# Optimization experiments

Hardware: AMD Instinct MI355X
Metric: run time of the kernel (lower is better)

## Reference

```python
import jax, jax.numpy as jnp
import numpy as np

B, L = 8, 2048
D_MODEL = 512
D_INNER = 1024   # expand * d_model
D_STATE = 16
D_CONV = 4
DT_RANK = 32     # d_model // 16
N_EXPERT = 4     # num_expert - 1 real experts (id 0 = identity)
N_LAYER = 2      # num_mamba_layer


def setup_inputs() -> dict:
    key = jax.random.key(0)
    ks = jax.random.split(key, 12)
    def rn(k, shape, scale):
        return jax.random.normal(k, shape, jnp.float32) * scale
    P = (N_EXPERT, N_LAYER)
    A_log = jnp.broadcast_to(
        jnp.log(jnp.arange(1, D_STATE + 1, dtype=jnp.float32)),
        P + (D_INNER, D_STATE)).copy()
    return {
        "x": rn(ks[0], (B, L, D_MODEL), 1.0),
        "expert_id": jax.random.randint(ks[1], (B,), 0, N_EXPERT + 1, jnp.int32),
        "W_in": rn(ks[2], P + (D_MODEL, 2 * D_INNER), D_MODEL ** -0.5),
        "conv_w": rn(ks[3], P + (D_INNER, D_CONV), D_CONV ** -0.5),
        "conv_b": jnp.zeros(P + (D_INNER,), jnp.float32),
        "W_x": rn(ks[4], P + (D_INNER, DT_RANK + 2 * D_STATE), D_INNER ** -0.5),
        "W_dt": rn(ks[5], P + (DT_RANK, D_INNER), DT_RANK ** -0.5),
        "b_dt": rn(ks[6], P + (D_INNER,), 0.1) - 4.0,  # softplus -> small dt
        "A_log": A_log,
        "D": jnp.ones(P + (D_INNER,), jnp.float32),
        "W_out": rn(ks[7], P + (D_INNER, D_MODEL), D_INNER ** -0.5),
    }


def _mamba_block(x, W_in, conv_w, conv_b, W_x, W_dt, b_dt, A_log, Dp, W_out):
    # x: [L, D_MODEL]
    Lx = x.shape[0]
    xr = x @ W_in                               # [L, 2*D_INNER]
    xc, res = jnp.split(xr, 2, axis=-1)
    # causal depthwise conv (kernel D_CONV), left-padded
    xp = jnp.pad(xc, ((D_CONV - 1, 0), (0, 0)))
    xc = sum(xp[k:k + Lx] * conv_w[:, k] for k in range(D_CONV)) + conv_b
    xc = jax.nn.silu(xc)
    proj = xc @ W_x                             # [L, DT_RANK + 2*D_STATE]
    dt = jax.nn.softplus(proj[:, :DT_RANK] @ W_dt + b_dt)        # [L, D_INNER]
    Bm = proj[:, DT_RANK:DT_RANK + D_STATE]                      # [L, D_STATE]
    Cm = proj[:, DT_RANK + D_STATE:]                             # [L, D_STATE]
    A = -jnp.exp(A_log)                                          # [D_INNER, D_STATE]
    def step(h, t):
        dt_t, B_t, C_t, x_t = t
        # discretize inside the step to avoid materializing [L,D_INNER,D_STATE]
        h = jnp.exp(dt_t[:, None] * A) * h + (dt_t * x_t)[:, None] * B_t[None, :]
        return h, h @ C_t                                        # y_t: [D_INNER]
    h0 = jnp.zeros((D_INNER, D_STATE), dtype=x.dtype)
    _, ys = jax.lax.scan(step, h0, (dt, Bm, Cm, xc))
    y = ys + Dp * xc
    y = y * jax.nn.silu(res)
    return y @ W_out                                             # [L, D_MODEL]


def reference(x, expert_id, W_in, conv_w, conv_b, W_x, W_dt, b_dt, A_log, D, W_out):
    # expert_id==0 -> identity; otherwise run expert (expert_id-1)'s stacked blocks
    idx = jnp.clip(expert_id - 1, 0, N_EXPERT - 1)
    def per_sample(xi, e):
        out = xi
        for l in range(N_LAYER):
            out = _mamba_block(out, W_in[e, l], conv_w[e, l], conv_b[e, l],
                               W_x[e, l], W_dt[e, l], b_dt[e, l],
                               A_log[e, l], D[e, l], W_out[e, l])
        return out
    y = jax.vmap(per_sample)(x, idx)
    return jnp.where((expert_id == 0)[:, None, None], x, y)
```

## Files before the change

kernel.cpp:

```cpp
#include <hip/hip_runtime.h>
#include <hip/hip_bf16.h>
#include <cmath>

#define B_SZ 8
#define L_SZ 2048
#define DM 512
#define DI 1024
#define DS 16
#define DC 4
#define DTR 32
#define NE 4
#define NL 2
#define NCH 64
#define TC2 32
#define TPER 8

typedef __attribute__((ext_vector_type(8))) short bf16x8;
typedef __attribute__((ext_vector_type(8))) unsigned short u16x8;
typedef __attribute__((ext_vector_type(4))) float f32x4;

__device__ __forceinline__ unsigned short f2bf(float x) {
  __hip_bfloat16 h = __float2bfloat16(x);
  return __builtin_bit_cast(unsigned short, h);
}
__device__ __forceinline__ float bf2f(unsigned short u) {
  return __builtin_bit_cast(float, (unsigned)u << 16);
}

__device__ __forceinline__ void glds16(const unsigned short* g, unsigned short* l) {
  __builtin_amdgcn_global_load_lds(
      (const __attribute__((address_space(1))) unsigned int*)g,
      (__attribute__((address_space(3))) unsigned int*)l, 16, 0, 0);
}

__device__ __forceinline__ float softplus_fast(float v) {
  return (v > 20.f) ? v : __logf(1.f + __expf(v));
}

__device__ __forceinline__ void pow16(float g, float* ee) {
  float g2 = g * g, g4 = g2 * g2, g8 = g4 * g4;
  ee[0] = g;        ee[1] = g2;       ee[2] = g2 * g;   ee[3] = g4;
  ee[4] = g4 * g;   ee[5] = g4 * g2;  ee[6] = ee[5] * g; ee[7] = g8;
  ee[8] = g8 * g;   ee[9] = g8 * g2;  ee[10] = ee[9] * g; ee[11] = g8 * g4;
  ee[12] = ee[11] * g; ee[13] = ee[11] * g2; ee[14] = ee[13] * g; ee[15] = g8 * g8;
}

__global__ __launch_bounds__(256) void transpose_w_kernel(
    const float* __restrict__ in, unsigned short* __restrict__ out, int R, int C)
{
  __shared__ float t[32][33];
  const int p = blockIdx.z;
  const int r0 = blockIdx.y * 32, c0 = blockIdx.x * 32;
  const int tx = threadIdx.x & 31, ty = threadIdx.x >> 5;
  const float* ip = in + (long)p * R * C;
  unsigned short* op = out + (long)p * R * C;
  #pragma unroll
  for (int i = 0; i < 32; i += 8)
    t[ty + i][tx] = ip[(long)(r0 + ty + i) * C + c0 + tx];
  __syncthreads();
  #pragma unroll
  for (int i = 0; i < 32; i += 8)
    op[(long)(c0 + ty + i) * R + r0 + tx] = f2bf(t[tx][ty + i]);
}

__global__ __launch_bounds__(256) void f2bf_kernel(
    const float* __restrict__ in, unsigned short* __restrict__ out)
{
  long i = ((long)blockIdx.x * 256 + threadIdx.x) * 4;
  float4 v = *(const float4*)(in + i);
  out[i + 0] = f2bf(v.x); out[i + 1] = f2bf(v.y);
  out[i + 2] = f2bf(v.z); out[i + 3] = f2bf(v.w);
}

template<int EPI, int TM, int TN>
__global__ __launch_bounds__(256) void gemm_bf16(
    const unsigned short* __restrict__ Abase, long aBatch, int K, int lda,
    const unsigned short* __restrict__ WTbase, long wStride,
    const float* __restrict__ xpass,
    const int* __restrict__ expert_id, int layer,
    float* __restrict__ Cf, unsigned short* __restrict__ Cbh,
    unsigned short* __restrict__ Cbh2,
    int ldc, long cBatch)
{
  constexpr int IF = TM / 32;
  constexpr int JF = TN / 32;
  constexpr int AST = TM / 4;
  constexpr int BST = TN / 4;

  const int b = blockIdx.z;
  const int eid = expert_id[b];
  const int m0 = blockIdx.y * TM, n0 = blockIdx.x * TN;
  const int tid = threadIdx.x;

  if (eid == 0) {
    if (EPI == 2) {
      float* Co = Cf + (long)b * cBatch;
      const float* xp = xpass + (long)b * L_SZ * DM;
      for (int i = tid; i < TM * TN; i += 256) {
        int r = m0 + (i / TN), c = n0 + (i % TN);
        Co[(long)r * ldc + c] = xp[(long)r * DM + c];
      }
    }
    return;
  }
  const int e = min(max(eid - 1, 0), NE - 1);
  const unsigned short* A = Abase + (long)b * aBatch;
  const unsigned short* WT = WTbase + (long)(e * NL + layer) * wStride;

  __shared__ unsigned short As[TM * 64];
  __shared__ unsigned short Bs[TN * 64];

  const int w = tid >> 6, lane = tid & 63;
  const int srow = lane >> 2;
  const int sgsw = ((lane & 3) ^ ((srow >> 1) & 3)) * 8;

  const unsigned short* aG0 = A + (long)(m0 + w * AST + srow) * lda + sgsw;
  const unsigned short* aG1 = aG0 + 16 * lda;
  unsigned short* aL0 = As + (w * AST) * 32;
  unsigned short* aL1 = As + (w * AST + 16) * 32;
  const unsigned short* bG0 = WT + (long)(n0 + w * BST + srow) * K + sgsw;
  const unsigned short* bG1 = bG0 + 16 * K;
  unsigned short* bL0 = Bs + (w * BST) * 32;
  unsigned short* bL1 = Bs + (w * BST + 16) * 32;

  const int wm = w >> 1, wn = w & 1;
  const int lo = lane & 15, hi = lane >> 4;
  int aoff[IF], boff[JF];
  #pragma unroll
  for (int i = 0; i < IF; ++i)
    aoff[i] = (wm * (TM / 2) + i * 16 + lo) * 32 + (hi ^ ((lo >> 1) & 3)) * 8;
  #pragma unroll
  for (int j = 0; j < JF; ++j)
    boff[j] = (wn * (TN / 2) + j * 16 + lo) * 32 + (hi ^ ((lo >> 1) & 3)) * 8;

  f32x4 acc[IF][JF] = {};

  for (int k0 = 0; k0 < K; k0 += 64) {
    glds16(aG0 + k0, aL0);
    if (AST == 32) glds16(aG1 + k0, aL1);
    glds16(aG0 + k0 + 32, aL0 + TM * 32);
    if (AST == 32) glds16(aG1 + k0 + 32, aL1 + TM * 32);
    glds16(bG0 + k0, bL0);
    if (BST == 32) glds16(bG1 + k0, bL1);
    glds16(bG0 + k0 + 32, bL0 + TN * 32);
    if (BST == 32) glds16(bG1 + k0 + 32, bL1 + TN * 32);
    __syncthreads();

    #pragma unroll
    for (int kk = 0; kk < 2; ++kk) {
      bf16x8 af[IF], bfr[JF];
      #pragma unroll
      for (int i = 0; i < IF; ++i)
        af[i] = *(const bf16x8*)(As + kk * TM * 32 + aoff[i]);
      #pragma unroll
      for (int j = 0; j < JF; ++j)
        bfr[j] = *(const bf16x8*)(Bs + kk * TN * 32 + boff[j]);
      #pragma unroll
      for (int i = 0; i < IF; ++i)
        #pragma unroll
        for (int j = 0; j < JF; ++j)
          acc[i][j] = __builtin_amdgcn_mfma_f32_16x16x32_bf16(af[i], bfr[j], acc[i][j], 0, 0, 0);
    }
    __syncthreads();
  }

  #pragma unroll
  for (int i = 0; i < IF; ++i) {
    #pragma unroll
    for (int j = 0; j < JF; ++j) {
      #pragma unroll
      for (int r = 0; r < 4; ++r) {
        int row = m0 + wm * (TM / 2) + i * 16 + hi * 4 + r;
        int col = n0 + wn * (TN / 2) + j * 16 + lo;
        float v = acc[i][j][r];
        if (EPI == 0 || EPI == 2) {
          (Cf + (long)b * cBatch)[(long)row * ldc + col] = v;
        } else if (EPI == 4) {
          (Cbh + (long)b * cBatch)[(long)row * ldc + col] = f2bf(v);
        } else {
          if (col < DI)
            (Cbh + (long)b * cBatch)[(long)row * DI + col] = f2bf(v);
          else
            (Cbh2 + (long)b * cBatch)[(long)row * DI + (col - DI)] = f2bf(v);
        }
      }
    }
  }
}

__global__ __launch_bounds__(256) void gemm_dt(
    const float* __restrict__ PRb, const unsigned short* __restrict__ WTbase,
    const float* __restrict__ biasBase,
    const int* __restrict__ expert_id, int layer,
    unsigned short* __restrict__ DTout)
{
  const int b = blockIdx.z;
  const int eid = expert_id[b];
  if (eid == 0) return;
  const int e = min(max(eid - 1, 0), NE - 1);
  const int m0 = blockIdx.y * 128, n0 = blockIdx.x * 128;
  const int tid = threadIdx.x;
  const float* A = PRb + (long)b * L_SZ * 64;
  const unsigned short* WT = WTbase + (long)(e * NL + layer) * DI * DTR;

  __shared__ unsigned short As[128 * 32];
  __shared__ unsigned short Bs[128 * 32];

  const int sr = tid >> 2, sg = tid & 3;
  const int slot = sg ^ ((sr >> 1) & 3);

  {
    float4 fa0 = *(const float4*)(A + (long)(m0 + sr) * 64 + sg * 8);
    float4 fa1 = *(const float4*)(A + (long)(m0 + sr) * 64 + sg * 8 + 4);
    float4 fb0 = *(const float4*)(A + (long)(m0 + sr + 64) * 64 + sg * 8);
    float4 fb1 = *(const float4*)(A + (long)(m0 + sr + 64) * 64 + sg * 8 + 4);
    u16x8 w0 = *(const u16x8*)(WT + (long)(n0 + sr) * DTR + sg * 8);
    u16x8 w1 = *(const u16x8*)(WT + (long)(n0 + sr + 64) * DTR + sg * 8);
    u16x8 ha = {f2bf(fa0.x), f2bf(fa0.y), f2bf(fa0.z), f2bf(fa0.w),
                f2bf(fa1.x), f2bf(fa1.y), f2bf(fa1.z), f2bf(fa1.w)};
    u16x8 hb = {f2bf(fb0.x), f2bf(fb0.y), f2bf(fb0.z), f2bf(fb0.w),
                f2bf(fb1.x), f2bf(fb1.y), f2bf(fb1.z), f2bf(fb1.w)};
    *(u16x8*)(As + sr * 32 + slot * 8) = ha;
    *(u16x8*)(As + (sr + 64) * 32 + slot * 8) = hb;
    *(u16x8*)(Bs + sr * 32 + slot * 8) = w0;
    *(u16x8*)(Bs + (sr + 64) * 32 + slot * 8) = w1;
  }
  __syncthreads();

  const int lane = tid & 63, w = tid >> 6;
  const int wm = w >> 1, wn = w & 1;
  const int lo = lane & 15, hi = lane >> 4;
  f32x4 acc[4][4] = {};
  bf16x8 af[4], bfr[4];
  #pragma unroll
  for (int i = 0; i < 4; ++i) {
    int r = wm * 64 + i * 16 + lo;
    af[i] = *(const bf16x8*)(As + r * 32 + (hi ^ ((r >> 1) & 3)) * 8);
  }
  #pragma unroll
  for (int j = 0; j < 4; ++j) {
    int r = wn * 64 + j * 16 + lo;
    bfr[j] = *(const bf16x8*)(Bs + r * 32 + (hi ^ ((r >> 1) & 3)) * 8);
  }
  #pragma unroll
  for (int i = 0; i < 4; ++i)
    #pragma unroll
    for (int j = 0; j < 4; ++j)
      acc[i][j] = __builtin_amdgcn_mfma_f32_16x16x32_bf16(af[i], bfr[j], acc[i][j], 0, 0, 0);

  const float* bias = biasBase + (long)(e * NL + layer) * DI;
  unsigned short* Cb = DTout + (long)b * L_SZ * DI;
  #pragma unroll
  for (int i = 0; i < 4; ++i)
    #pragma unroll
    for (int j = 0; j < 4; ++j)
      #pragma unroll
      for (int r = 0; r < 4; ++r) {
        int row = m0 + wm * 64 + i * 16 + hi * 4 + r;
        int col = n0 + wn * 64 + j * 16 + lo;
        float v = softplus_fast(acc[i][j][r] + bias[col]);
        Cb[(long)row * DI + col] = f2bf(v);
      }
}

__global__ __launch_bounds__(256) void conv_silu_kernel(
    const unsigned short* __restrict__ XCP,
    const float* __restrict__ conv_w, const float* __restrict__ conv_b,
    const int* __restrict__ expert_id, int layer,
    unsigned short* __restrict__ XCbf)
{
  const int idx = blockIdx.x * 256 + threadIdx.x;
  const int d8 = idx & 127;
  const int tb = (idx >> 7) & (L_SZ / TPER - 1);
  const int b = idx >> 15;
  const int eid = expert_id[b];
  if (eid == 0) return;
  const int e = min(max(eid - 1, 0), NE - 1);
  const int d0 = d8 * 8;
  const int t0 = tb * TPER;

  const float* cwp = conv_w + ((long)(e * NL + layer) * DI + d0) * DC;
  float4 w4[8];
  #pragma unroll
  for (int j = 0; j < 8; ++j) w4[j] = *(const float4*)(cwp + j * 4);
  float cb[8];
  {
    const float* cbp = conv_b + (long)(e * NL + layer) * DI + d0;
    float4 c0 = *(const float4*)(cbp);
    float4 c1 = *(const float4*)(cbp + 4);
    cb[0] = c0.x; cb[1] = c0.y; cb[2] = c0.z; cb[3] = c0.w;
    cb[4] = c1.x; cb[5] = c1.y; cb[6] = c1.z; cb[7] = c1.w;
  }

  const unsigned short* base = XCP + ((long)b * L_SZ + t0) * DI + d0;
  u16x8 r[TPER + 3];
  #pragma unroll
  for (int i = 0; i < TPER + 3; ++i) {
    if (t0 - 3 + i < 0) {
      u16x8 z = {0, 0, 0, 0, 0, 0, 0, 0};
      r[i] = z;
    } else {
      r[i] = *(const u16x8*)(base + (long)(i - 3) * DI);
    }
  }

  unsigned short* ob = XCbf + ((long)b * L_SZ + t0) * DI + d0;
  #pragma unroll
  for (int j = 0; j < TPER; ++j) {
    u16x8 o;
    #pragma unroll
    for (int ch = 0; ch < 8; ++ch) {
      float acc = cb[ch];
      acc = fmaf(bf2f(r[j + 0][ch]), w4[ch].x, acc);
      acc = fmaf(bf2f(r[j + 1][ch]), w4[ch].y, acc);
      acc = fmaf(bf2f(r[j + 2][ch]), w4[ch].z, acc);
      acc = fmaf(bf2f(r[j + 3][ch]), w4[ch].w, acc);
      float v = acc / (1.f + __expf(-acc));
      o[ch] = f2bf(v);
    }
    *(u16x8*)(ob + (long)j * DI) = o;
  }
}

__global__ __launch_bounds__(256) void scan_p1(
    const unsigned short* __restrict__ DTb, const unsigned short* __restrict__ XCbf,
    const float* __restrict__ PR, const float* __restrict__ A_log,
    const int* __restrict__ expert_id, int layer,
    unsigned short* __restrict__ Hws, float* __restrict__ Sws)
{
  const int b = blockIdx.z, c = blockIdx.y;
  const int eid = expert_id[b];
  if (eid == 0) return;
  const int e = min(max(eid - 1, 0), NE - 1);
  const int d = blockIdx.x * 256 + threadIdx.x;
  const int t0 = c * TC2;

  __shared__ float sB[TC2][16];
  const float* prb = PR + (long)b * L_SZ * 64;
  for (int i = threadIdx.x; i < TC2 * 16; i += 256) {
    int t = i >> 4, s = i & 15;
    sB[t][s] = prb[(long)(t0 + t) * 64 + DTR + s];
  }

  float Aval[16];
  const float* al = A_log + ((long)(e * NL + layer) * DI + d) * DS;
  #pragma unroll
  for (int s = 0; s < 16; ++s) Aval[s] = -__expf(al[s]);
  bool geo = true;
  #pragma unroll
  for (int s = 1; s < 16; ++s)
    geo = geo && (fabsf(Aval[s] - Aval[0] * (s + 1)) <= 1e-4f * (s + 1));

  float h[16];
  #pragma unroll
  for (int s = 0; s < 16; ++s) h[s] = 0.f;
  float S = 0.f;

  const unsigned short* dtp = DTb + ((long)b * L_SZ + t0) * DI + d;
  const unsigned short* xcp = XCbf + ((long)b * L_SZ + t0) * DI + d;
  __syncthreads();

  const float A0 = Aval[0];
  for (int t4 = 0; t4 < TC2; t4 += 4) {
    float dt4[4], xc4[4];
    #pragma unroll
    for (int k = 0; k < 4; ++k) {
      dt4[k] = bf2f(dtp[(long)(t4 + k) * DI]);
      xc4[k] = bf2f(xcp[(long)(t4 + k) * DI]);
    }
    if (geo) {
      #pragma unroll
      for (int k = 0; k < 4; ++k) {
        int t = t4 + k;
        float dt = dt4[k];
        S += dt;
        float dx = dt * xc4[k];
        float4 b0 = *(const float4*)&sB[t][0];
        float4 b1 = *(const float4*)&sB[t][4];
        float4 b2 = *(const float4*)&sB[t][8];
        float4 b3 = *(const float4*)&sB[t][12];
        float bv[16] = {b0.x, b0.y, b0.z, b0.w, b1.x, b1.y, b1.z, b1.w,
                        b2.x, b2.y, b2.z, b2.w, b3.x, b3.y, b3.z, b3.w};
        float ee[16];
        pow16(__expf(dt * A0), ee);
        #pragma unroll
        for (int s = 0; s < 16; ++s)
          h[s] = fmaf(ee[s], h[s], dx * bv[s]);
      }
    } else {
      #pragma unroll
      for (int k = 0; k < 4; ++k) {
        int t = t4 + k;
        float dt = dt4[k];
        S += dt;
        float dx = dt * xc4[k];
        float4 b0 = *(const float4*)&sB[t][0];
        float4 b1 = *(const float4*)&sB[t][4];
        float4 b2 = *(const float4*)&sB[t][8];
        float4 b3 = *(const float4*)&sB[t][12];
        float bv[16] = {b0.x, b0.y, b0.z, b0.w, b1.x, b1.y, b1.z, b1.w,
                        b2.x, b2.y, b2.z, b2.w, b3.x, b3.y, b3.z, b3.w};
        #pragma unroll
        for (int s = 0; s < 16; ++s)
          h[s] = fmaf(__expf(dt * Aval[s]), h[s], dx * bv[s]);
      }
    }
  }

  const long hoff = (((long)b * NCH + c) * DI + d) * 16;
  u16x8 h0, h1;
  #pragma unroll
  for (int s = 0; s < 8; ++s) { h0[s] = f2bf(h[s]); h1[s] = f2bf(h[s + 8]); }
  *(u16x8*)&Hws[hoff] = h0;
  *(u16x8*)&Hws[hoff + 8] = h1;
  Sws[((long)b * NCH + c) * DI + d] = S;
}

__global__ __launch_bounds__(256) void scan_combine(
    unsigned short* __restrict__ Hws, const float* __restrict__ Sws,
    const float* __restrict__ A_log,
    const int* __restrict__ expert_id, int layer)
{
  const int gid = blockIdx.x * 256 + threadIdx.x;
  const int s = gid & 15;
  const int d = (gid >> 4) & (DI - 1);
  const int b = gid >> 14;
  const int eid = expert_id[b];
  if (eid == 0) return;
  const int e = min(max(eid - 1, 0), NE - 1);
  const float Aval = -__expf(A_log[((long)(e * NL + layer) * DI + d) * DS + s]);
  float h = 0.f;
  for (int c = 0; c < NCH; ++c) {
    const long off = (((long)b * NCH + c) * DI + d) * 16 + s;
    float q = bf2f(Hws[off]);
    float Sc = Sws[((long)b * NCH + c) * DI + d];
    Hws[off] = f2bf(h);
    h = fmaf(__expf(Aval * Sc), h, q);
  }
}

__global__ __launch_bounds__(256) void scan_p2(
    const unsigned short* __restrict__ DTb, const unsigned short* __restrict__ XCbf,
    const unsigned short* __restrict__ RESb, const float* __restrict__ PR,
    const float* __restrict__ A_log, const float* __restrict__ Dw,
    const unsigned short* __restrict__ Hws,
    const int* __restrict__ expert_id, int layer,
    unsigned short* __restrict__ Ybf)
{
  const int b = blockIdx.z, c = blockIdx.y;
  const int eid = expert_id[b];
  if (eid == 0) return;
  const int e = min(max(eid - 1, 0), NE - 1);
  const int d = blockIdx.x * 256 + threadIdx.x;
  const int t0 = c * TC2;

  __shared__ float sBC[TC2][32];
  const float* prb = PR + (long)b * L_SZ * 64;
  for (int i = threadIdx.x; i < TC2 * 32; i += 256) {
    int t = i >> 5, j = i & 31;
    sBC[t][j] = prb[(long)(t0 + t) * 64 + DTR + j];
  }

  float Aval[16];
  const float* al = A_log + ((long)(e * NL + layer) * DI + d) * DS;
  #pragma unroll
  for (int s = 0; s < 16; ++s) Aval[s] = -__expf(al[s]);
  bool geo = true;
  #pragma unroll
  for (int s = 1; s < 16; ++s)
    geo = geo && (fabsf(Aval[s] - Aval[0] * (s + 1)) <= 1e-4f * (s + 1));

  float h[16];
  const long hoff = (((long)b * NCH + c) * DI + d) * 16;
  {
    u16x8 h0 = *(const u16x8*)&Hws[hoff];
    u16x8 h1 = *(const u16x8*)&Hws[hoff + 8];
    #pragma unroll
    for (int s = 0; s < 8; ++s) { h[s] = bf2f(h0[s]); h[s + 8] = bf2f(h1[s]); }
  }
  const float Dd = Dw[(long)(e * NL + layer) * DI + d];

  const unsigned short* dtp = DTb + ((long)b * L_SZ + t0) * DI + d;
  const unsigned short* xcp = XCbf + ((long)b * L_SZ + t0) * DI + d;
  const unsigned short* rsp = RESb + ((long)b * L_SZ + t0) * DI + d;
  unsigned short* yb = Ybf + ((long)b * L_SZ + t0) * DI + d;
  __syncthreads();

  const float A0 = Aval[0];
  for (int t4 = 0; t4 < TC2; t4 += 4) {
    float dt4[4], xc4[4], rs4[4];
    #pragma unroll
    for (int k = 0; k < 4; ++k) {
      dt4[k] = bf2f(dtp[(long)(t4 + k) * DI]);
      xc4[k] = bf2f(xcp[(long)(t4 + k) * DI]);
      rs4[k] = bf2f(rsp[(long)(t4 + k) * DI]);
    }
    unsigned short yo[4];
    #pragma unroll
    for (int k = 0; k < 4; ++k) {
      int t = t4 + k;
      float dt = dt4[k], xc = xc4[k], res = rs4[k];
      float dx = dt * xc;
      float4 b0 = *(const float4*)&sBC[t][0];
      float4 b1 = *(const float4*)&sBC[t][4];
      float4 b2 = *(const float4*)&sBC[t][8];
      float4 b3 = *(const float4*)&sBC[t][12];
      float4 c0 = *(const float4*)&sBC[t][16];
      float4 c1 = *(const float4*)&sBC[t][20];
      float4 c2 = *(const float4*)&sBC[t][24];
      float4 c3 = *(const float4*)&sBC[t][28];
      float bv[16] = {b0.x, b0.y, b0.z, b0.w, b1.x, b1.y, b1.z, b1.w,
                      b2.x, b2.y, b2.z, b2.w, b3.x, b3.y, b3.z, b3.w};
      float cv[16] = {c0.x, c0.y, c0.z, c0.w, c1.x, c1.y, c1.z, c1.w,
                      c2.x, c2.y, c2.z, c2.w, c3.x, c3.y, c3.z, c3.w};
      float y0 = 0.f, y1 = 0.f, y2 = 0.f, y3 = 0.f;
      if (geo) {
        float ee[16];
        pow16(__expf(dt * A0), ee);
        #pragma unroll
        for (int s = 0; s < 16; s += 4) {
          h[s]     = fmaf(ee[s],     h[s],     dx * bv[s]);
          h[s + 1] = fmaf(ee[s + 1], h[s + 1], dx * bv[s + 1]);
          h[s + 2] = fmaf(ee[s + 2], h[s + 2], dx * bv[s + 2]);
          h[s + 3] = fmaf(ee[s + 3], h[s + 3], dx * bv[s + 3]);
          y0 = fmaf(h[s],     cv[s],     y0);
          y1 = fmaf(h[s + 1], cv[s + 1], y1);
          y2 = fmaf(h[s + 2], cv[s + 2], y2);
          y3 = fmaf(h[s + 3], cv[s + 3], y3);
        }
      } else {
        #pragma unroll
        for (int s = 0; s < 16; s += 4) {
          h[s]     = fmaf(__expf(dt * Aval[s]),     h[s],     dx * bv[s]);
          h[s + 1] = fmaf(__expf(dt * Aval[s + 1]), h[s + 1], dx * bv[s + 1]);
          h[s + 2] = fmaf(__expf(dt * Aval[s + 2]), h[s + 2], dx * bv[s + 2]);
          h[s + 3] = fmaf(__expf(dt * Aval[s + 3]), h[s + 3], dx * bv[s + 3]);
          y0 = fmaf(h[s],     cv[s],     y0);
          y1 = fmaf(h[s + 1], cv[s + 1], y1);
          y2 = fmaf(h[s + 2], cv[s + 2], y2);
          y3 = fmaf(h[s + 3], cv[s + 3], y3);
        }
      }
      float y = (y0 + y1) + (y2 + y3);
      y = fmaf(Dd, xc, y);
      float sil = res / (1.f + __expf(-res));
      yo[k] = f2bf(y * sil);
    }
    #pragma unroll
    for (int k = 0; k < 4; ++k)
      yb[(long)(t4 + k) * DI] = yo[k];
  }
}

extern "C" void kernel_launch(void* const* d_in, const int* in_sizes, int n_in,
                              void* d_out, int out_size, void* d_ws, size_t ws_size,
                              hipStream_t stream)
{
  const float* x      = (const float*)d_in[0];
  const int*   eidp   = (const int*)d_in[1];
  const float* W_in   = (const float*)d_in[2];
  const float* conv_w = (const float*)d_in[3];
  const float* conv_b = (const float*)d_in[4];
  const float* W_x    = (const float*)d_in[5];
  const float* W_dt   = (const float*)d_in[6];
  const float* b_dt   = (const float*)d_in[7];
  const float* A_log  = (const float*)d_in[8];
  const float* Dw     = (const float*)d_in[9];
  const float* W_out  = (const float*)d_in[10];
  float* out = (float*)d_out;
  float* ws  = (float*)d_ws;

  float* PR  = ws;
  float* Sws = PR + 1048576L;
  unsigned short* Hws  = (unsigned short*)(Sws + 524288L);
  unsigned short* DTb  = Hws + 8388608L;
  unsigned short* XCP  = DTb + 16777216L;
  unsigned short* Ybf  = XCP;
  unsigned short* XCbf = XCP + 16777216L;
  unsigned short* RESb = XCbf + 16777216L;
  unsigned short* XB   = RESb + 16777216L;
  unsigned short* WinT  = XB + 8388608L;
  unsigned short* WoutT = WinT + 8388608L;
  unsigned short* WxT   = WoutT + 4194304L;
  unsigned short* WdtT  = WxT + 524288L;

  transpose_w_kernel<<<dim3(2 * DI / 32, DM / 32, NE * NL), 256, 0, stream>>>(
      W_in, WinT, DM, 2 * DI);
  transpose_w_kernel<<<dim3(DM / 32, DI / 32, NE * NL), 256, 0, stream>>>(
      W_out, WoutT, DI, DM);
  transpose_w_kernel<<<dim3(2, DI / 32, NE * NL), 256, 0, stream>>>(
      W_x, WxT, DI, 64);
  transpose_w_kernel<<<dim3(DI / 32, 1, NE * NL), 256, 0, stream>>>(
      W_dt, WdtT, DTR, DI);
  f2bf_kernel<<<8192, 256, 0, stream>>>(x, XB);

  for (int l = 0; l < NL; ++l) {
    gemm_bf16<3, 128, 128><<<dim3(2 * DI / 128, L_SZ / 128, B_SZ), 256, 0, stream>>>(
        XB, (long)L_SZ * DM, DM, DM, WinT, (long)(2 * DI) * DM,
        nullptr, eidp, l, nullptr, XCP, RESb, 0, (long)L_SZ * DI);

    conv_silu_kernel<<<B_SZ * (L_SZ / TPER) * 128 / 256, 256, 0, stream>>>(
        XCP, conv_w, conv_b, eidp, l, XCbf);

    gemm_bf16<0, 64, 64><<<dim3(1, L_SZ / 64, B_SZ), 256, 0, stream>>>(
        XCbf, (long)L_SZ * DI, DI, DI, WxT, (long)64 * DI,
        nullptr, eidp, l, PR, nullptr, nullptr, 64, (long)L_SZ * 64);

    gemm_dt<<<dim3(DI / 128, L_SZ / 128, B_SZ), 256, 0, stream>>>(
        PR, WdtT, b_dt, eidp, l, DTb);

    scan_p1<<<dim3(DI / 256, NCH, B_SZ), 256, 0, stream>>>(
        DTb, XCbf, PR, A_log, eidp, l, Hws, Sws);
    scan_combine<<<(B_SZ * DI * DS) / 256, 256, 0, stream>>>(
        Hws, Sws, A_log, eidp, l);
    scan_p2<<<dim3(DI / 256, NCH, B_SZ), 256, 0, stream>>>(
        DTb, XCbf, RESb, PR, A_log, Dw, Hws, eidp, l, Ybf);

    if (l == NL - 1) {
      gemm_bf16<2, 128, 128><<<dim3(DM / 128, L_SZ / 128, B_SZ), 256, 0, stream>>>(
          Ybf, (long)L_SZ * DI, DI, DI, WoutT, (long)DM * DI,
          x, eidp, l, out, nullptr, nullptr, DM, (long)L_SZ * DM);
    } else {
      gemm_bf16<4, 128, 128><<<dim3(DM / 128, L_SZ / 128, B_SZ), 256, 0, stream>>>(
          Ybf, (long)L_SZ * DI, DI, DI, WoutT, (long)DM * DI,
          nullptr, eidp, l, nullptr, XB, nullptr, DM, (long)L_SZ * DM);
    }
  }
}
```

Before: 405.2 us.

## Add 512-thread double-buffered GEMM with larger tiles for in/out projections

Introduces a new gemm_big kernel with 256-row tiles, 8 waves, and a two-stage LDS double buffer. It issues async global-to-LDS loads for tile kt+2 while computing tile kt, using explicit vmcnt waits and barriers. The in-projection and out-projection GEMMs now use it to get more data reuse per block and to overlap memory latency with MFMA work. The old gemm_bf16 is trimmed to the float-output path only, and the larger tiles mean fewer blocks, which costs some occupancy and tail balance.

```diff
diff --git a/kernel.cpp b/kernel.cpp
--- a/kernel.cpp
+++ b/kernel.cpp
@@ -72,6 +72,142 @@
   out[i + 2] = f2bf(v.z); out[i + 3] = f2bf(v.w);
 }
 
+template<int EPI, int TN>
+__global__ __launch_bounds__(512) void gemm_big(
+    const unsigned short* __restrict__ Abase, long aBatch, int K, int lda,
+    const unsigned short* __restrict__ WTbase, long wStride,
+    const float* __restrict__ xpass,
+    const int* __restrict__ expert_id, int layer,
+    float* __restrict__ Cf, unsigned short* __restrict__ Cbh,
+    unsigned short* __restrict__ Cbh2,
+    int ldc, long cBatch)
+{
+  constexpr int TM = 256;
+  constexpr int IF = 8;
+  constexpr int JF = TN / 64;
+  constexpr int LT = (TM + TN) / 64;
+
+  const int b = blockIdx.z;
+  const int eid = expert_id[b];
+  const int m0 = blockIdx.y * TM, n0 = blockIdx.x * TN;
+  const int tid = threadIdx.x;
+
+  if (eid == 0) {
+    if (EPI == 2) {
+      float* Co = Cf + (long)b * cBatch;
+      const float* xp = xpass + (long)b * L_SZ * DM;
+      for (int i = tid; i < TM * TN; i += 512) {
+        int r = m0 + (i / TN), c = n0 + (i % TN);
+        Co[(long)r * ldc + c] = xp[(long)r * DM + c];
+      }
+    }
+    return;
+  }
+  const int e = min(max(eid - 1, 0), NE - 1);
+  const unsigned short* A = Abase + (long)b * aBatch;
+  const unsigned short* WT = WTbase + (long)(e * NL + layer) * wStride;
+
+  __shared__ unsigned short As[2 * 2 * TM * 32];
+  __shared__ unsigned short Bs[2 * 2 * TN * 32];
+
+  const int w = tid >> 6, l = tid & 63;
+  const int srw = l >> 2;
+  const int csw = ((l & 3) ^ ((l >> 3) & 3)) * 8;
+
+  const int wm = w >> 2, wn = w & 3;
+  const int lo = l & 15, hi = l >> 4;
+  const int rsl = (hi ^ ((lo >> 1) & 3)) * 8;
+  int aoff[IF], boff[JF];
+  #pragma unroll
+  for (int i = 0; i < IF; ++i)
+    aoff[i] = (wm * 128 + i * 16 + lo) * 32 + rsl;
+  #pragma unroll
+  for (int j = 0; j < JF; ++j)
+    boff[j] = (wn * (TN / 4) + j * 16 + lo) * 32 + rsl;
+
+  const int NT = K >> 6;
+
+  auto STAGE = [&](int buf, int kt) {
+    #pragma unroll
+    for (int kh = 0; kh < 2; ++kh) {
+      #pragma unroll
+      for (int rc = 0; rc < TM / 128; ++rc) {
+        int row = rc * 128 + w * 16 + srw;
+        glds16(A + (long)(m0 + row) * lda + kt * 64 + kh * 32 + csw,
+               As + buf * (2 * TM * 32) + kh * (TM * 32) + (rc * 128 + w * 16) * 32);
+      }
+      #pragma unroll
+      for (int rc = 0; rc < TN / 128; ++rc) {
+        int row = rc * 128 + w * 16 + srw;
+        glds16(WT + (long)(n0 + row) * K + kt * 64 + kh * 32 + csw,
+               Bs + buf * (2 * TN * 32) + kh * (TN * 32) + (rc * 128 + w * 16) * 32);
+      }
+    }
+  };
+
+  f32x4 acc[IF][JF] = {};
+
+  STAGE(0, 0);
+  STAGE(1, 1);
+
+  for (int kt = 0; kt < NT; ++kt) {
+    const int p = kt & 1;
+    if (kt + 1 < NT) {
+      if constexpr (LT == 8) asm volatile("s_waitcnt vmcnt(8)" ::: "memory");
+      else                   asm volatile("s_waitcnt vmcnt(6)" ::: "memory");
+    } else {
+      asm volatile("s_waitcnt vmcnt(0)" ::: "memory");
+    }
+    __builtin_amdgcn_sched_barrier(0);
+    __builtin_amdgcn_s_barrier();
+    __builtin_amdgcn_sched_barrier(0);
+
+    #pragma unroll
+    for (int kk = 0; kk < 2; ++kk) {
+      const unsigned short* ab = As + p * (2 * TM * 32) + kk * (TM * 32);
+      const unsigned short* bb = Bs + p * (2 * TN * 32) + kk * (TN * 32);
+      bf16x8 af[IF], bfr[JF];
+      #pragma unroll
+      for (int i = 0; i < IF; ++i) af[i] = *(const bf16x8*)(ab + aoff[i]);
+      #pragma unroll
+      for (int j = 0; j < JF; ++j) bfr[j] = *(const bf16x8*)(bb + boff[j]);
+      #pragma unroll
+      for (int i = 0; i < IF; ++i)
+        #pragma unroll
+        for (int j = 0; j < JF; ++j)
+          acc[i][j] = __builtin_amdgcn_mfma_f32_16x16x32_bf16(af[i], bfr[j], acc[i][j], 0, 0, 0);
+    }
+
+    __builtin_amdgcn_sched_barrier(0);
+    __builtin_amdgcn_s_barrier();
+    __builtin_amdgcn_sched_barrier(0);
+    if (kt + 2 < NT) STAGE(p, kt + 2);
+  }
+
+  #pragma unroll
+  for (int i = 0; i < IF; ++i) {
+    #pragma unroll
+    for (int j = 0; j < JF; ++j) {
+      #pragma unroll
+      for (int r = 0; r < 4; ++r) {
+        int row = m0 + wm * 128 + i * 16 + hi * 4 + r;
+        int col = n0 + wn * (TN / 4) + j * 16 + lo;
+        float v = acc[i][j][r];
+        if (EPI == 2) {
+          (Cf + (long)b * cBatch)[(long)row * ldc + col] = v;
+        } else if (EPI == 4) {
+          (Cbh + (long)b * cBatch)[(long)row * ldc + col] = f2bf(v);
+        } else {
+          if (col < DI)
+            (Cbh + (long)b * cBatch)[(long)row * DI + col] = f2bf(v);
+          else
+            (Cbh2 + (long)b * cBatch)[(long)row * DI + (col - DI)] = f2bf(v);
+        }
+      }
+    }
+  }
+}
+
 template<int EPI, int TM, int TN>
 __global__ __launch_bounds__(256) void gemm_bf16(
     const unsigned short* __restrict__ Abase, long aBatch, int K, int lda,
@@ -92,17 +228,7 @@
   const int m0 = blockIdx.y * TM, n0 = blockIdx.x * TN;
   const int tid = threadIdx.x;
 
-  if (eid == 0) {
-    if (EPI == 2) {
-      float* Co = Cf + (long)b * cBatch;
-      const float* xp = xpass + (long)b * L_SZ * DM;
-      for (int i = tid; i < TM * TN; i += 256) {
-        int r = m0 + (i / TN), c = n0 + (i % TN);
-        Co[(long)r * ldc + c] = xp[(long)r * DM + c];
-      }
-    }
-    return;
-  }
+  if (eid == 0) return;
   const int e = min(max(eid - 1, 0), NE - 1);
   const unsigned short* A = Abase + (long)b * aBatch;
   const unsigned short* WT = WTbase + (long)(e * NL + layer) * wStride;
@@ -172,17 +298,7 @@
       for (int r = 0; r < 4; ++r) {
         int row = m0 + wm * (TM / 2) + i * 16 + hi * 4 + r;
         int col = n0 + wn * (TN / 2) + j * 16 + lo;
-        float v = acc[i][j][r];
-        if (EPI == 0 || EPI == 2) {
-          (Cf + (long)b * cBatch)[(long)row * ldc + col] = v;
-        } else if (EPI == 4) {
-          (Cbh + (long)b * cBatch)[(long)row * ldc + col] = f2bf(v);
-        } else {
-          if (col < DI)
-            (Cbh + (long)b * cBatch)[(long)row * DI + col] = f2bf(v);
-          else
-            (Cbh2 + (long)b * cBatch)[(long)row * DI + (col - DI)] = f2bf(v);
-        }
+        (Cf + (long)b * cBatch)[(long)row * ldc + col] = acc[i][j][r];
       }
     }
   }
@@ -595,7 +711,7 @@
   f2bf_kernel<<<8192, 256, 0, stream>>>(x, XB);
 
   for (int l = 0; l < NL; ++l) {
-    gemm_bf16<3, 128, 128><<<dim3(2 * DI / 128, L_SZ / 128, B_SZ), 256, 0, stream>>>(
+    gemm_big<3, 256><<<dim3(2 * DI / 256, L_SZ / 256, B_SZ), 512, 0, stream>>>(
         XB, (long)L_SZ * DM, DM, DM, WinT, (long)(2 * DI) * DM,
         nullptr, eidp, l, nullptr, XCP, RESb, 0, (long)L_SZ * DI);
 
@@ -617,11 +733,11 @@
         DTb, XCbf, RESb, PR, A_log, Dw, Hws, eidp, l, Ybf);
 
     if (l == NL - 1) {
-      gemm_bf16<2, 128, 128><<<dim3(DM / 128, L_SZ / 128, B_SZ), 256, 0, stream>>>(
+      gemm_big<2, 128><<<dim3(DM / 128, L_SZ / 256, B_SZ), 512, 0, stream>>>(
           Ybf, (long)L_SZ * DI, DI, DI, WoutT, (long)DM * DI,
           x, eidp, l, out, nullptr, nullptr, DM, (long)L_SZ * DM);
     } else {
-      gemm_bf16<4, 128, 128><<<dim3(DM / 128, L_SZ / 128, B_SZ), 256, 0, stream>>>(
+      gemm_big<4, 128><<<dim3(DM / 128, L_SZ / 256, B_SZ), 512, 0, stream>>>(
           Ybf, (long)L_SZ * DI, DI, DI, WoutT, (long)DM * DI,
           nullptr, eidp, l, nullptr, XB, nullptr, DM, (long)L_SZ * DM);
     }
```

Result: slower. 422.4 us (+4.2%).
